# Kernel tuning notes

Hardware: AMD Instinct MI355X
Metric: run time of the kernel (lower is better)

## Reference

```python
import jax, jax.numpy as jnp
import numpy as np

N = 100000   # nodes
E = 1600000  # edges
D = 64       # hidden_channels == out_channels
L = 3        # num_layers
EPS = 1e-5
SCALE = 1.0 / float(np.sqrt(D))


def setup_inputs() -> dict:
    key = jax.random.key(0)
    ks = jax.random.split(key, 12)
    x = jax.random.normal(ks[0], (N, D), dtype=jnp.float32)
    edge_index = jax.random.randint(ks[1], (2, E), 0, N, dtype=jnp.int32)
    s = 0.1
    Wq = jax.random.normal(ks[2], (L, D, D), dtype=jnp.float32) * s
    Wk = jax.random.normal(ks[3], (L, D, D), dtype=jnp.float32) * s
    Wv = jax.random.normal(ks[4], (L, D, D), dtype=jnp.float32) * s
    Ws = jax.random.normal(ks[5], (L, D, D), dtype=jnp.float32) * s
    bq = jax.random.normal(ks[6], (L, D), dtype=jnp.float32) * s
    bk = jax.random.normal(ks[7], (L, D), dtype=jnp.float32) * s
    bv = jax.random.normal(ks[8], (L, D), dtype=jnp.float32) * s
    bs = jax.random.normal(ks[9], (L, D), dtype=jnp.float32) * s
    gamma = jnp.ones((L, D), dtype=jnp.float32)
    beta = jnp.zeros((L, D), dtype=jnp.float32)
    return {"x": x, "edge_index": edge_index, "Wq": Wq, "bq": bq,
            "Wk": Wk, "bk": bk, "Wv": Wv, "bv": bv, "Ws": Ws, "bs": bs,
            "gamma": gamma, "beta": beta}


def layer_norm(h, g, b):
    mu = h.mean(-1, keepdims=True)
    var = ((h - mu) ** 2).mean(-1, keepdims=True)
    return (h - mu) * jax.lax.rsqrt(var + EPS) * g + b


def transformer_conv(x, src, dst, Wq, bq, Wk, bk, Wv, bv, Ws, bs):
    # PyG TransformerConv, heads=1, concat=True, root_weight=True, beta=False
    q = x @ Wq + bq            # [N, D]
    k = x @ Wk + bk            # [N, D]
    v = x @ Wv + bv            # [N, D]
    # per-edge attention logit: <q_dst, k_src> / sqrt(D)
    score = jnp.einsum('ed,ed->e', q[dst], k[src]) * SCALE  # [E]
    # segment softmax over incoming edges of each dst node
    m = jax.ops.segment_max(score, dst, num_segments=N)     # [N]
    e = jnp.exp(score - m[dst])                             # [E]
    denom = jax.ops.segment_sum(e, dst, num_segments=N)     # [N]
    alpha = e / denom[dst]                                  # [E]
    agg = jax.ops.segment_sum(alpha[:, None] * v[src], dst, num_segments=N)  # [N, D]
    return agg + x @ Ws + bs   # root/skip connection


def reference(x, edge_index, Wq, bq, Wk, bk, Wv, bv, Ws, bs, gamma, beta):
    src, dst = edge_index[0], edge_index[1]
    x_init = None
    for i in range(L):
        h = transformer_conv(x, src, dst, Wq[i], bq[i], Wk[i], bk[i],
                             Wv[i], bv[i], Ws[i], bs[i])
        h = jax.nn.relu(h)
        if i == 0:
            x_init = h
        else:
            h = h + x_init
        x = layer_norm(h, gamma[i], beta[i])
    return x
```

## Files before the change

kernel.cpp:

```cpp
#include <hip/hip_runtime.h>
#include <math.h>

#define NN 100000
#define EE 1600000
#define EPS 1e-5f
#define SCALEF 0.125f

#define NB 1024
#define BCAP 2688
#define CH 4096

typedef __attribute__((ext_vector_type(4))) float f32x4;
typedef __attribute__((ext_vector_type(8))) short bf16x8;
typedef __attribute__((ext_vector_type(8))) unsigned short u16x8;

__device__ __forceinline__ unsigned short f2bf_rne(float f) {
    unsigned u = __builtin_bit_cast(unsigned, f);
    u += 0x7FFFu + ((u >> 16) & 1u);
    return (unsigned short)(u >> 16);
}
__device__ __forceinline__ float bf2f(unsigned short h) {
    return __builtin_bit_cast(float, ((unsigned)h) << 16);
}
__device__ __forceinline__ int dot4(int a, int b, int c) {
#if __has_builtin(__builtin_amdgcn_sdot4)
    return __builtin_amdgcn_sdot4(a, b, c, false);
#else
    int r = c;
#pragma unroll
    for (int i = 0; i < 4; i++)
        r += ((int)(char)(a >> (8 * i)) & ~0) * ((int)(char)(b >> (8 * i)));
    return r;
#endif
}


__global__ __launch_bounds__(256) void bin_edges2(const int* __restrict__ ei,
                                                  int* __restrict__ bcnt,
                                                  unsigned* __restrict__ bbuf, int E) {
    __shared__ int hist[NB];
    __shared__ int gbase[NB];
    __shared__ int cur[NB];
    int base = blockIdx.x * CH;
    int tid = threadIdx.x;

    for (int i = tid; i < NB; i += 256) { hist[i] = 0; cur[i] = 0; }
    __syncthreads();

    for (int i = tid; i < CH; i += 256) {
        int e = base + i;
        if (e < E) atomicAdd(&hist[ei[E + e] >> 7], 1);
    }
    __syncthreads();

    for (int i = tid; i < NB; i += 256)
        gbase[i] = hist[i] ? atomicAdd(&bcnt[i], hist[i]) : 0;
    __syncthreads();

    for (int i = tid; i < CH; i += 256) {
        int e = base + i;
        if (e < E) {
            int s = ei[e];
            int d = ei[E + e];
            int b = d >> 7;
            int pos = gbase[b] + atomicAdd(&cur[b], 1);
            if (pos < BCAP) bbuf[b * BCAP + pos] = ((unsigned)s << 7) | (unsigned)(d & 127);
        }
    }
}

__global__ __launch_bounds__(1024) void scan_buckets(const int* __restrict__ bcnt,
                                                     int* __restrict__ bbase) {
    __shared__ int sh[1024];
    int tid = threadIdx.x;
    int v = bcnt[tid];
    sh[tid] = v;
    __syncthreads();
    for (int off = 1; off < 1024; off <<= 1) {
        int t = (tid >= off) ? sh[tid - off] : 0;
        __syncthreads();
        sh[tid] += t;
        __syncthreads();
    }
    bbase[tid] = sh[tid] - v;
}

__global__ __launch_bounds__(256) void bucket_csr(const unsigned* __restrict__ bbuf,
                                                  const int* __restrict__ bcnt,
                                                  const int* __restrict__ bbase,
                                                  int* __restrict__ iOff,
                                                  int* __restrict__ csr, int N) {
    __shared__ unsigned ed[BCAP];
    __shared__ int hist[128], excl[128], cur[128];
    int b = blockIdx.x;
    int tid = threadIdx.x;
    int cnt = min(bcnt[b], BCAP);
    int base = bbase[b];

    for (int i = tid; i < cnt; i += 256) ed[i] = bbuf[b * BCAP + i];
    if (tid < 128) { hist[tid] = 0; cur[tid] = 0; }
    __syncthreads();
    for (int i = tid; i < cnt; i += 256) atomicAdd(&hist[ed[i] & 127], 1);
    __syncthreads();
    if (tid < 128) excl[tid] = hist[tid];
    __syncthreads();
    for (int off = 1; off < 128; off <<= 1) {
        int t = (tid < 128 && tid >= off) ? excl[tid - off] : 0;
        __syncthreads();
        if (tid < 128) excl[tid] += t;
        __syncthreads();
    }
    if (tid < 128) {
        int ex = excl[tid] - hist[tid];
        excl[tid] = ex;
        int node = b * 128 + tid;
        if (node <= N) iOff[node] = base + ex;
    }
    __syncthreads();
    for (int i = tid; i < cnt; i += 256) {
        unsigned pk = ed[i];
        int ld = pk & 127;
        int pos = atomicAdd(&cur[ld], 1);
        csr[base + excl[ld] + pos] = (int)(pk >> 7);
    }
}


__global__ __launch_bounds__(64) void wfrag_prep(
    const float* __restrict__ Wq, const float* __restrict__ Wk,
    const float* __restrict__ Wv, const float* __restrict__ Ws,
    unsigned short* __restrict__ fragH, unsigned short* __restrict__ fragL)
{
    int bm = blockIdx.x;
    int layer = bm >> 2, m = bm & 3;
    const float* W = ((m == 0) ? Wq : (m == 1) ? Wk : (m == 2) ? Wv : Ws) + layer * 4096;
    int l = threadIdx.x;
    int colb = l & 15, kg = l >> 4;
#pragma unroll
    for (int ks = 0; ks < 2; ks++)
#pragma unroll
        for (int ct = 0; ct < 4; ct++) {
            size_t base = ((((size_t)bm * 2 + ks) * 4 + ct) * 64 + l) * 8;
#pragma unroll
            for (int e = 0; e < 8; e++) {
                int kk = ks * 32 + kg * 8 + e;
                int col = ct * 16 + colb;
                float f = W[kk * 64 + col];
                unsigned short h = f2bf_rne(f);
                fragH[base + e] = h;
                fragL[base + e] = f2bf_rne(f - bf2f(h));
            }
        }
}


__global__ __launch_bounds__(256) void gemm4_mfma(const void* __restrict__ xp, int xbf, int N,
    const unsigned short* __restrict__ fragH, const unsigned short* __restrict__ fragL,
    int layer,
    const float* __restrict__ bq, const float* __restrict__ bk,
    const float* __restrict__ bv, const float* __restrict__ bs,
    unsigned short* __restrict__ oq, unsigned char* __restrict__ kv8,
    float* __restrict__ sc, unsigned short* __restrict__ os)
{
    __shared__ unsigned short xhi[64][80];
    __shared__ unsigned short xlo[64][80];

    int tid = threadIdx.x;
    int row0 = blockIdx.x * 64;

    if (xbf) {
        const unsigned short* xb = (const unsigned short*)xp;
#pragma unroll
        for (int i = 0; i < 2; i++) {
            int idx = tid + i * 256;
            int r = idx >> 3;
            int c8 = (idx & 7) * 8;
            u16x8 u = {0, 0, 0, 0, 0, 0, 0, 0};
            if (row0 + r < N) u = *(const u16x8*)&xb[(size_t)(row0 + r) * 64 + c8];
            *(u16x8*)&xhi[r][c8] = u;
        }
    } else {
        const float* xf = (const float*)xp;
#pragma unroll
        for (int i = 0; i < 4; i++) {
            int idx = tid + i * 256;
            int r = idx >> 4;
            int c4 = (idx & 15) * 4;
            f32x4 f = {0.f, 0.f, 0.f, 0.f};
            if (row0 + r < N) f = *(const f32x4*)&xf[(size_t)(row0 + r) * 64 + c4];
            ushort4 hh, ll;
            unsigned short h;
            h = f2bf_rne(f.x); hh.x = h; ll.x = f2bf_rne(f.x - bf2f(h));
            h = f2bf_rne(f.y); hh.y = h; ll.y = f2bf_rne(f.y - bf2f(h));
            h = f2bf_rne(f.z); hh.z = h; ll.z = f2bf_rne(f.z - bf2f(h));
            h = f2bf_rne(f.w); hh.w = h; ll.w = f2bf_rne(f.w - bf2f(h));
            *(ushort4*)&xhi[r][c4] = hh;
            *(ushort4*)&xlo[r][c4] = ll;
        }
    }
    __syncthreads();

    int w = tid >> 6, l = tid & 63;
    int colb = l & 15, kg = l >> 4;
    int bm = layer * 4 + w;
    const float* bias = (w == 0) ? bq : (w == 1) ? bk : (w == 2) ? bv : bs;

    bf16x8 bh[2][4], bl[2][4];
#pragma unroll
    for (int ks = 0; ks < 2; ks++)
#pragma unroll
        for (int ct = 0; ct < 4; ct++) {
            size_t fb = ((((size_t)bm * 2 + ks) * 4 + ct) * 64 + l) * 8;
            bh[ks][ct] = *(const bf16x8*)&fragH[fb];
            bl[ks][ct] = *(const bf16x8*)&fragL[fb];
        }

    f32x4 acc[4][4] = {};
#pragma unroll
    for (int rt = 0; rt < 4; rt++) {
        int r = rt * 16 + colb;
#pragma unroll
        for (int ks = 0; ks < 2; ks++) {
            bf16x8 ah = *(const bf16x8*)&xhi[r][ks * 32 + kg * 8];
#pragma unroll
            for (int ct = 0; ct < 4; ct++) {
                acc[rt][ct] = __builtin_amdgcn_mfma_f32_16x16x32_bf16(ah, bh[ks][ct], acc[rt][ct], 0, 0, 0);
                acc[rt][ct] = __builtin_amdgcn_mfma_f32_16x16x32_bf16(ah, bl[ks][ct], acc[rt][ct], 0, 0, 0);
            }
            if (!xbf) {
                bf16x8 al = *(const bf16x8*)&xlo[r][ks * 32 + kg * 8];
#pragma unroll
                for (int ct = 0; ct < 4; ct++)
                    acc[rt][ct] = __builtin_amdgcn_mfma_f32_16x16x32_bf16(al, bh[ks][ct], acc[rt][ct], 0, 0, 0);
            }
        }
    }

    float bias4[4];
#pragma unroll
    for (int ct = 0; ct < 4; ct++) bias4[ct] = bias[ct * 16 + colb];
#pragma unroll
    for (int rt = 0; rt < 4; rt++)
#pragma unroll
        for (int ct = 0; ct < 4; ct++)
#pragma unroll
            for (int j = 0; j < 4; j++) acc[rt][ct][j] += bias4[ct];

    if (w == 0 || w == 3) {
        unsigned short* dst = (w == 0) ? oq : os;
#pragma unroll
        for (int rt = 0; rt < 4; rt++)
#pragma unroll
            for (int j = 0; j < 4; j++) {
                int gr = row0 + rt * 16 + kg * 4 + j;
                if (gr < N) {
                    ushort4 pk;
                    pk.x = f2bf_rne(acc[rt][0][j]);
                    pk.y = f2bf_rne(acc[rt][1][j]);
                    pk.z = f2bf_rne(acc[rt][2][j]);
                    pk.w = f2bf_rne(acc[rt][3][j]);
                    *(ushort4*)&dst[(size_t)gr * 64 + colb * 4] = pk;
                }
            }
    } else if (w == 1) {
#pragma unroll
        for (int rt = 0; rt < 4; rt++)
#pragma unroll
            for (int j = 0; j < 4; j++) {
                int gr = row0 + rt * 16 + kg * 4 + j;
                float a0 = acc[rt][0][j], a1 = acc[rt][1][j];
                float a2 = acc[rt][2][j], a3 = acc[rt][3][j];
                float m = fmaxf(fmaxf(fabsf(a0), fabsf(a1)), fmaxf(fabsf(a2), fabsf(a3)));
                m = fmaxf(m, __shfl_xor(m, 1));
                m = fmaxf(m, __shfl_xor(m, 2));
                m = fmaxf(m, __shfl_xor(m, 4));
                m = fmaxf(m, __shfl_xor(m, 8));
                m = fmaxf(m, 1e-20f);
                float rs = 127.f / m;
                unsigned pk;
                pk  = (unsigned)((int)rintf(a0 * rs) & 0xff);
                pk |= (unsigned)((int)rintf(a1 * rs) & 0xff) << 8;
                pk |= (unsigned)((int)rintf(a2 * rs) & 0xff) << 16;
                pk |= (unsigned)((int)rintf(a3 * rs) & 0xff) << 24;
                if (gr < N) {
                    *(unsigned*)(kv8 + (size_t)gr * 128 + colb * 4) = pk;
                    if (colb == 0) sc[gr * 2] = m * (1.f / 127.f);
                }
            }
    } else {
#pragma unroll
        for (int rt = 0; rt < 4; rt++)
#pragma unroll
            for (int j = 0; j < 4; j++) {
                int gr = row0 + rt * 16 + kg * 4 + j;
                float a0 = acc[rt][0][j], a1 = acc[rt][1][j];
                float a2 = acc[rt][2][j], a3 = acc[rt][3][j];
                float m = fmaxf(fmaxf(fabsf(a0), fabsf(a1)), fmaxf(fabsf(a2), fabsf(a3)));
                m = fmaxf(m, __shfl_xor(m, 1));
                m = fmaxf(m, __shfl_xor(m, 2));
                m = fmaxf(m, __shfl_xor(m, 4));
                m = fmaxf(m, __shfl_xor(m, 8));
                m = fmaxf(m, 1e-20f);
                float rs = 127.f / m;
                unsigned pk;
                pk  = (unsigned)((int)rintf(a0 * rs) + 128);
                pk |= (unsigned)((int)rintf(a1 * rs) + 128) << 8;
                pk |= (unsigned)((int)rintf(a2 * rs) + 128) << 16;
                pk |= (unsigned)((int)rintf(a3 * rs) + 128) << 24;
                if (gr < N) {
                    *(unsigned*)(kv8 + (size_t)gr * 128 + 64 + colb * 4) = pk;
                    if (colb == 0) sc[gr * 2 + 1] = m * (1.f / 127.f);
                }
            }
    }
}


__global__ __launch_bounds__(256) void node_attn(
    const int* __restrict__ off, const int* __restrict__ csr,
    const unsigned short* __restrict__ q, const unsigned char* __restrict__ kv8,
    const float* __restrict__ sc, const unsigned short* __restrict__ xs,
    const float* __restrict__ gamma, const float* __restrict__ beta,
    unsigned short* __restrict__ xinit, unsigned short* __restrict__ xoutb,
    float* __restrict__ outf, int layer, int N)
{
    int node = (blockIdx.x * blockDim.x + threadIdx.x) >> 3;
    int sl = threadIdx.x & 7;
    if (node >= N) return;
    int e0 = off[node], e1 = off[node + 1];
    size_t nb = (size_t)node * 64 + sl * 8;

    u16x8 qu = *(const u16x8*)&q[nb];
    float qf[8];
#pragma unroll
    for (int i = 0; i < 8; i++) qf[i] = bf2f((unsigned short)qu[i]);
    float am = 0.f;
#pragma unroll
    for (int i = 0; i < 8; i++) am = fmaxf(am, fabsf(qf[i]));
    am = fmaxf(am, __shfl_xor(am, 1));
    am = fmaxf(am, __shfl_xor(am, 2));
    am = fmaxf(am, __shfl_xor(am, 4));
    am = fmaxf(am, 1e-20f);
    float qrs = 127.f / am;
    unsigned qlo = 0, qhi = 0;
#pragma unroll
    for (int i = 0; i < 4; i++)
        qlo |= (unsigned)((int)rintf(qf[i] * qrs) & 0xff) << (8 * i);
#pragma unroll
    for (int i = 0; i < 4; i++)
        qhi |= (unsigned)((int)rintf(qf[4 + i] * qrs) & 0xff) << (8 * i);
    const float qC = am * (1.f / 127.f) * SCALEF * 1.44269504f;

    float ssum = 0.f, s128 = 0.f;
    float a0 = 0.f, a1 = 0.f, a2 = 0.f, a3 = 0.f;
    float a4 = 0.f, a5 = 0.f, a6 = 0.f, a7 = 0.f;

#define EDGE(ks, vs, kk, vv)                                                \
    {                                                                       \
        int t = dot4((int)kk.y, (int)qhi, dot4((int)kk.x, (int)qlo, 0));    \
        t += __shfl_xor(t, 1); t += __shfl_xor(t, 2); t += __shfl_xor(t, 4);\
        float d = (float)t * ks * qC;                                       \
        float p = __builtin_amdgcn_exp2f(d);                                \
        ssum += p;                                                          \
        float pp = p * vs;                                                  \
        s128 += pp;                                                         \
        a0 += pp * (float)(vv.x & 0xffu);                                   \
        a1 += pp * (float)((vv.x >> 8) & 0xffu);                            \
        a2 += pp * (float)((vv.x >> 16) & 0xffu);                           \
        a3 += pp * (float)(vv.x >> 24);                                     \
        a4 += pp * (float)(vv.y & 0xffu);                                   \
        a5 += pp * (float)((vv.y >> 8) & 0xffu);                            \
        a6 += pp * (float)((vv.y >> 16) & 0xffu);                           \
        a7 += pp * (float)(vv.y >> 24);                                     \
    }

    int e = e0;
    for (; e + 3 < e1; e += 4) {
        int s0 = csr[e + 0], s1 = csr[e + 1], s2 = csr[e + 2], s3 = csr[e + 3];
        const unsigned char* r0 = kv8 + (size_t)s0 * 128 + sl * 8;
        const unsigned char* r1 = kv8 + (size_t)s1 * 128 + sl * 8;
        const unsigned char* r2 = kv8 + (size_t)s2 * 128 + sl * 8;
        const unsigned char* r3 = kv8 + (size_t)s3 * 128 + sl * 8;
        uint2 k0 = *(const uint2*)r0, v0 = *(const uint2*)(r0 + 64);
        uint2 k1 = *(const uint2*)r1, v1 = *(const uint2*)(r1 + 64);
        uint2 k2 = *(const uint2*)r2, v2 = *(const uint2*)(r2 + 64);
        uint2 k3 = *(const uint2*)r3, v3 = *(const uint2*)(r3 + 64);
        float2 c0 = *(const float2*)&sc[s0 * 2];
        float2 c1 = *(const float2*)&sc[s1 * 2];
        float2 c2 = *(const float2*)&sc[s2 * 2];
        float2 c3 = *(const float2*)&sc[s3 * 2];
        EDGE(c0.x, c0.y, k0, v0);
        EDGE(c1.x, c1.y, k1, v1);
        EDGE(c2.x, c2.y, k2, v2);
        EDGE(c3.x, c3.y, k3, v3);
    }
    for (; e < e1; e++) {
        int s0 = csr[e];
        const unsigned char* r0 = kv8 + (size_t)s0 * 128 + sl * 8;
        uint2 k0 = *(const uint2*)r0, v0 = *(const uint2*)(r0 + 64);
        float2 c0 = *(const float2*)&sc[s0 * 2];
        EDGE(c0.x, c0.y, k0, v0);
    }

    float inv = (e1 > e0) ? 1.f / ssum : 0.f;
    float corr = 128.f * s128;
    u16x8 sku = *(const u16x8*)&xs[nb];
    float h[8];
    h[0] = fmaxf((a0 - corr) * inv + bf2f((unsigned short)sku[0]), 0.f);
    h[1] = fmaxf((a1 - corr) * inv + bf2f((unsigned short)sku[1]), 0.f);
    h[2] = fmaxf((a2 - corr) * inv + bf2f((unsigned short)sku[2]), 0.f);
    h[3] = fmaxf((a3 - corr) * inv + bf2f((unsigned short)sku[3]), 0.f);
    h[4] = fmaxf((a4 - corr) * inv + bf2f((unsigned short)sku[4]), 0.f);
    h[5] = fmaxf((a5 - corr) * inv + bf2f((unsigned short)sku[5]), 0.f);
    h[6] = fmaxf((a6 - corr) * inv + bf2f((unsigned short)sku[6]), 0.f);
    h[7] = fmaxf((a7 - corr) * inv + bf2f((unsigned short)sku[7]), 0.f);

    if (layer == 0) {
        u16x8 hu;
#pragma unroll
        for (int i = 0; i < 8; i++) hu[i] = (short)f2bf_rne(h[i]);
        *(u16x8*)&xinit[nb] = hu;
    } else {
        u16x8 xi = *(const u16x8*)&xinit[nb];
#pragma unroll
        for (int i = 0; i < 8; i++) h[i] += bf2f((unsigned short)xi[i]);
    }

    float s1 = 0.f;
#pragma unroll
    for (int i = 0; i < 8; i++) s1 += h[i];
    s1 += __shfl_xor(s1, 1); s1 += __shfl_xor(s1, 2); s1 += __shfl_xor(s1, 4);
    float mu = s1 * (1.f / 64.f);
    float dd[8], s2 = 0.f;
#pragma unroll
    for (int i = 0; i < 8; i++) { dd[i] = h[i] - mu; s2 += dd[i] * dd[i]; }
    s2 += __shfl_xor(s2, 1); s2 += __shfl_xor(s2, 2); s2 += __shfl_xor(s2, 4);
    float rs = rsqrtf(s2 * (1.f / 64.f) + EPS);

    size_t nb0 = (size_t)node * 64;
#pragma unroll
    for (int j = 0; j < 4; j++) {
        int dim = 16 * j + 2 * sl;
        float2 g2 = *(const float2*)&gamma[dim];
        float2 b2 = *(const float2*)&beta[dim];
        float olo = dd[j] * rs * g2.x + b2.x;
        float ohi = dd[4 + j] * rs * g2.y + b2.y;
        if (layer == 2) {
            float2 o2 = {olo, ohi};
            *(float2*)&outf[nb0 + dim] = o2;
        } else {
            ushort2 o2;
            o2.x = f2bf_rne(olo);
            o2.y = f2bf_rne(ohi);
            *(ushort2*)&xoutb[nb0 + dim] = o2;
        }
    }
}


extern "C" void kernel_launch(void* const* d_in, const int* in_sizes, int n_in,
                              void* d_out, int out_size, void* d_ws, size_t ws_size,
                              hipStream_t stream) {
    const float* x     = (const float*)d_in[0];
    const int*   ei    = (const int*)d_in[1];
    const float* Wq    = (const float*)d_in[2];
    const float* bq    = (const float*)d_in[3];
    const float* Wk    = (const float*)d_in[4];
    const float* bk    = (const float*)d_in[5];
    const float* Wv    = (const float*)d_in[6];
    const float* bv    = (const float*)d_in[7];
    const float* Wsk   = (const float*)d_in[8];
    const float* bsk   = (const float*)d_in[9];
    const float* gamma = (const float*)d_in[10];
    const float* beta  = (const float*)d_in[11];
    float* out = (float*)d_out;

    const int N = NN, E = EE;
    const size_t ND = (size_t)N * 64;

    char* p = (char*)d_ws;
    unsigned short* fQ  = (unsigned short*)p; p += ND * 2;
    unsigned short* fS  = (unsigned short*)p; p += ND * 2;
    unsigned short* fI  = (unsigned short*)p; p += ND * 2;
    unsigned char*  fKV = (unsigned char*)p;  p += ND * 2;
    float* fSC = (float*)p; p += (size_t)N * 2 * 4;
    int* iOff = (int*)p;  p += (size_t)(N + 1) * 4;
    int* bcnt = (int*)p;  p += NB * 4;
    int* bbase = (int*)p; p += NB * 4;
    int* iSrc = (int*)p;  p += (size_t)E * 4;
    unsigned short* fragH = (unsigned short*)p; p += (size_t)12 * 2 * 4 * 64 * 8 * 2;
    unsigned short* fragL = (unsigned short*)p; p += (size_t)12 * 2 * 4 * 64 * 8 * 2;
    unsigned* bbuf = (unsigned*)fS;

    hipMemsetAsync(bcnt, 0, NB * 4, stream);
    bin_edges2<<<(E + CH - 1) / CH, 256, 0, stream>>>(ei, bcnt, bbuf, E);
    wfrag_prep<<<12, 64, 0, stream>>>(Wq, Wk, Wv, Wsk, fragH, fragL);
    scan_buckets<<<1, 1024, 0, stream>>>(bcnt, bbase);
    bucket_csr<<<NB, 256, 0, stream>>>(bbuf, bcnt, bbase, iOff, iSrc, N);

    for (int l = 0; l < 3; l++) {
        const void* xin = (l == 0) ? (const void*)x : (const void*)fQ;
        gemm4_mfma<<<(N + 63) / 64, 256, 0, stream>>>(xin, (l == 0) ? 0 : 1, N,
            fragH, fragL, l,
            bq + l * 64, bk + l * 64, bv + l * 64, bsk + l * 64,
            fQ, fKV, fSC, fS);
        node_attn<<<(N * 8 + 255) / 256, 256, 0, stream>>>(iOff, iSrc, fQ, fKV, fSC, fS,
            gamma + l * 64, beta + l * 64, fI, fQ, out, l, N);
    }
}
```

Before: 286.8 us.

## Interleave int8 K/V per lane, shrink scales to bf16, prefetch CSR indices

The K and V int8 rows are interleaved so each lane fetches its 8 K bytes and 8 V bytes in one 16-byte load instead of two 8-byte loads. The per-node K/V dequant scales are stored as a packed bf16 pair, so one 4-byte load replaces a float2 load. In the edge loop the next four CSR source indices are loaded before the current batch is processed, to hide the dependent-load latency of the gather. The bf16 scales lose some precision in the attention logits and values.

Result: faster. 274.9 us (median of 2 runs) (-4.1%).

```diff
diff --git a/kernel.cpp b/kernel.cpp
--- a/kernel.cpp
+++ b/kernel.cpp
@@ -29,7 +29,7 @@
     int r = c;
 #pragma unroll
     for (int i = 0; i < 4; i++)
-        r += ((int)(char)(a >> (8 * i)) & ~0) * ((int)(char)(b >> (8 * i)));
+        r += ((int)(char)(a >> (8 * i))) * ((int)(char)(b >> (8 * i)));
     return r;
 #endif
 }
@@ -160,7 +160,7 @@
     const float* __restrict__ bq, const float* __restrict__ bk,
     const float* __restrict__ bv, const float* __restrict__ bs,
     unsigned short* __restrict__ oq, unsigned char* __restrict__ kv8,
-    float* __restrict__ sc, unsigned short* __restrict__ os)
+    unsigned short* __restrict__ sc16, unsigned short* __restrict__ os)
 {
     __shared__ unsigned short xhi[64][80];
     __shared__ unsigned short xlo[64][80];
@@ -283,8 +283,8 @@
                 pk |= (unsigned)((int)rintf(a2 * rs) & 0xff) << 16;
                 pk |= (unsigned)((int)rintf(a3 * rs) & 0xff) << 24;
                 if (gr < N) {
-                    *(unsigned*)(kv8 + (size_t)gr * 128 + colb * 4) = pk;
-                    if (colb == 0) sc[gr * 2] = m * (1.f / 127.f);
+                    *(unsigned*)(kv8 + (size_t)gr * 128 + colb * 8) = pk;
+                    if (colb == 0) sc16[gr * 2] = f2bf_rne(m * (1.f / 127.f));
                 }
             }
     } else {
@@ -308,8 +308,8 @@
                 pk |= (unsigned)((int)rintf(a2 * rs) + 128) << 16;
                 pk |= (unsigned)((int)rintf(a3 * rs) + 128) << 24;
                 if (gr < N) {
-                    *(unsigned*)(kv8 + (size_t)gr * 128 + 64 + colb * 4) = pk;
-                    if (colb == 0) sc[gr * 2 + 1] = m * (1.f / 127.f);
+                    *(unsigned*)(kv8 + (size_t)gr * 128 + colb * 8 + 4) = pk;
+                    if (colb == 0) sc16[gr * 2 + 1] = f2bf_rne(m * (1.f / 127.f));
                 }
             }
     }
@@ -319,7 +319,7 @@
 __global__ __launch_bounds__(256) void node_attn(
     const int* __restrict__ off, const int* __restrict__ csr,
     const unsigned short* __restrict__ q, const unsigned char* __restrict__ kv8,
-    const float* __restrict__ sc, const unsigned short* __restrict__ xs,
+    const unsigned short* __restrict__ sc16, const unsigned short* __restrict__ xs,
     const float* __restrict__ gamma, const float* __restrict__ beta,
     unsigned short* __restrict__ xinit, unsigned short* __restrict__ xoutb,
     float* __restrict__ outf, int layer, int N)
@@ -355,51 +355,57 @@
     float a0 = 0.f, a1 = 0.f, a2 = 0.f, a3 = 0.f;
     float a4 = 0.f, a5 = 0.f, a6 = 0.f, a7 = 0.f;
 
-#define EDGE(ks, vs, kk, vv)                                                \
+#define EDGE(cc, uu)                                                        \
     {                                                                       \
-        int t = dot4((int)kk.y, (int)qhi, dot4((int)kk.x, (int)qlo, 0));    \
+        float ks = __builtin_bit_cast(float, cc << 16);                     \
+        float vs = __builtin_bit_cast(float, cc & 0xffff0000u);             \
+        int t = dot4((int)uu.z, (int)qhi, dot4((int)uu.x, (int)qlo, 0));    \
         t += __shfl_xor(t, 1); t += __shfl_xor(t, 2); t += __shfl_xor(t, 4);\
         float d = (float)t * ks * qC;                                       \
         float p = __builtin_amdgcn_exp2f(d);                                \
         ssum += p;                                                          \
         float pp = p * vs;                                                  \
         s128 += pp;                                                         \
-        a0 += pp * (float)(vv.x & 0xffu);                                   \
-        a1 += pp * (float)((vv.x >> 8) & 0xffu);                            \
-        a2 += pp * (float)((vv.x >> 16) & 0xffu);                           \
-        a3 += pp * (float)(vv.x >> 24);                                     \
-        a4 += pp * (float)(vv.y & 0xffu);                                   \
-        a5 += pp * (float)((vv.y >> 8) & 0xffu);                            \
-        a6 += pp * (float)((vv.y >> 16) & 0xffu);                           \
-        a7 += pp * (float)(vv.y >> 24);                                     \
+        a0 += pp * (float)(uu.y & 0xffu);                                   \
+        a1 += pp * (float)((uu.y >> 8) & 0xffu);                            \
+        a2 += pp * (float)((uu.y >> 16) & 0xffu);                           \
+        a3 += pp * (float)(uu.y >> 24);                                     \
+        a4 += pp * (float)(uu.w & 0xffu);                                   \
+        a5 += pp * (float)((uu.w >> 8) & 0xffu);                            \
+        a6 += pp * (float)((uu.w >> 16) & 0xffu);                           \
+        a7 += pp * (float)(uu.w >> 24);                                     \
     }
 
     int e = e0;
-    for (; e + 3 < e1; e += 4) {
-        int s0 = csr[e + 0], s1 = csr[e + 1], s2 = csr[e + 2], s3 = csr[e + 3];
-        const unsigned char* r0 = kv8 + (size_t)s0 * 128 + sl * 8;
-        const unsigned char* r1 = kv8 + (size_t)s1 * 128 + sl * 8;
-        const unsigned char* r2 = kv8 + (size_t)s2 * 128 + sl * 8;
-        const unsigned char* r3 = kv8 + (size_t)s3 * 128 + sl * 8;
-        uint2 k0 = *(const uint2*)r0, v0 = *(const uint2*)(r0 + 64);
-        uint2 k1 = *(const uint2*)r1, v1 = *(const uint2*)(r1 + 64);
-        uint2 k2 = *(const uint2*)r2, v2 = *(const uint2*)(r2 + 64);
-        uint2 k3 = *(const uint2*)r3, v3 = *(const uint2*)(r3 + 64);
-        float2 c0 = *(const float2*)&sc[s0 * 2];
-        float2 c1 = *(const float2*)&sc[s1 * 2];
-        float2 c2 = *(const float2*)&sc[s2 * 2];
-        float2 c3 = *(const float2*)&sc[s3 * 2];
-        EDGE(c0.x, c0.y, k0, v0);
-        EDGE(c1.x, c1.y, k1, v1);
-        EDGE(c2.x, c2.y, k2, v2);
-        EDGE(c3.x, c3.y, k3, v3);
+    if (e + 3 < e1) {
+        int np0 = csr[e], np1 = csr[e + 1], np2 = csr[e + 2], np3 = csr[e + 3];
+        for (; e + 3 < e1; ) {
+            int s0 = np0, s1 = np1, s2 = np2, s3 = np3;
+            uint4 u0 = *(const uint4*)(kv8 + (size_t)s0 * 128 + sl * 16);
+            uint4 u1 = *(const uint4*)(kv8 + (size_t)s1 * 128 + sl * 16);
+            uint4 u2 = *(const uint4*)(kv8 + (size_t)s2 * 128 + sl * 16);
+            uint4 u3 = *(const uint4*)(kv8 + (size_t)s3 * 128 + sl * 16);
+            unsigned c0 = *(const unsigned*)&sc16[s0 * 2];
+            unsigned c1 = *(const unsigned*)&sc16[s1 * 2];
+            unsigned c2 = *(const unsigned*)&sc16[s2 * 2];
+            unsigned c3 = *(const unsigned*)&sc16[s3 * 2];
+            e += 4;
+            int t1 = e1 - 1;
+            np0 = csr[min(e, t1)];
+            np1 = csr[min(e + 1, t1)];
+            np2 = csr[min(e + 2, t1)];
+            np3 = csr[min(e + 3, t1)];
+            EDGE(c0, u0);
+            EDGE(c1, u1);
+            EDGE(c2, u2);
+            EDGE(c3, u3);
+        }
     }
     for (; e < e1; e++) {
         int s0 = csr[e];
-        const unsigned char* r0 = kv8 + (size_t)s0 * 128 + sl * 8;
-        uint2 k0 = *(const uint2*)r0, v0 = *(const uint2*)(r0 + 64);
-        float2 c0 = *(const float2*)&sc[s0 * 2];
-        EDGE(c0.x, c0.y, k0, v0);
+        uint4 u0 = *(const uint4*)(kv8 + (size_t)s0 * 128 + sl * 16);
+        unsigned c0 = *(const unsigned*)&sc16[s0 * 2];
+        EDGE(c0, u0);
     }
 
     float inv = (e1 > e0) ? 1.f / ssum : 0.f;
@@ -483,7 +489,7 @@
     unsigned short* fS  = (unsigned short*)p; p += ND * 2;
     unsigned short* fI  = (unsigned short*)p; p += ND * 2;
     unsigned char*  fKV = (unsigned char*)p;  p += ND * 2;
-    float* fSC = (float*)p; p += (size_t)N * 2 * 4;
+    unsigned short* fSC = (unsigned short*)p; p += (size_t)N * 2 * 2;
     int* iOff = (int*)p;  p += (size_t)(N + 1) * 4;
     int* bcnt = (int*)p;  p += NB * 4;
     int* bbase = (int*)p; p += NB * 4;
```
